# Kernel optimization log

Measured on AMD Instinct MI355X. Metric: run time of the kernel, lower is better.

Reference implementation:

```python
import jax, jax.numpy as jnp
import numpy as np

WINDOW = 2048
STEP = WINDOW // 2                 # 1024
N_SAMPLES = 131072
N_COEFFS = WINDOW // 2 + 1         # 1025
N_FRAMES = N_SAMPLES // STEP       # 128
Z_DIM = 128
BATCH, N_EVENTS, IMP_SAMPLES = 64, 1, 4096
BASE_RES = 0.02
RES_RANGE = (1.0 - BASE_RES) * 0.99


def setup_inputs() -> dict:
    key = jax.random.key(0)
    k1, k2, k3 = jax.random.split(key, 3)
    z = jax.random.normal(k1, (BATCH, N_EVENTS, Z_DIM), dtype=jnp.float32)
    impulse = jax.random.normal(k2, (BATCH, N_EVENTS, IMP_SAMPLES), dtype=jnp.float32)
    # stand-in for ConvUpsample: linear z -> (n_coeffs * n_frames)
    W_tf = jax.random.normal(k3, (Z_DIM, N_COEFFS * N_FRAMES), dtype=jnp.float32) * 0.02
    b_tf = jnp.zeros((N_COEFFS * N_FRAMES,), dtype=jnp.float32)
    return {"z": z, "impulse": impulse, "W_tf": W_tf, "b_tf": b_tf}


def _hann(n):
    # periodic hann (torch.hann_window default)
    return (0.5 - 0.5 * jnp.cos(2.0 * jnp.pi * jnp.arange(n) / n)).astype(jnp.float32)


def reference(z, impulse, W_tf, b_tf):
    B, E, imp_len = impulse.shape
    pad = N_SAMPLES - imp_len + WINDOW
    x = jnp.pad(impulse, ((0, 0), (0, 0), (0, pad)))  # (B,E,n_samples+window)
    win = _hann(WINDOW)

    # windowed_audio: overlapping frames * hann window -> (B,E,F,W)
    idx = jnp.arange(N_FRAMES)[:, None] * STEP + jnp.arange(WINDOW)[None, :]
    windowed = x[..., idx] * win

    # transfer functions: linear, reshape (C,F) -> transpose to (F,C), squash
    tf = (z.reshape(-1, Z_DIM) @ W_tf + b_tf).reshape(B, E, N_COEFFS, N_FRAMES)
    tf = jnp.transpose(tf, (0, 1, 3, 2))                       # (B,E,F,C)
    tf = BASE_RES + jax.nn.sigmoid(tf) * RES_RANGE

    cur_specs = jnp.fft.rfft(windowed, axis=-1)                # (B,E,F,C) complex64

    # advance_one_frame rotation: [re,im] @ [[c,-s],[s,-c]]
    g = jnp.linspace(0.0, np.pi, N_COEFFS).astype(jnp.float32)
    c, s = jnp.cos(g), jnp.sin(g)

    def step(prev_audio, inp):
        cur_spec, tfi = inp
        ps = jnp.fft.rfft(prev_audio, axis=-1)
        re, im = ps.real, ps.imag
        rot = jax.lax.complex(re * c + im * s, -(re * s + im * c))
        spec = (cur_spec + rot) * tfi
        audio = jnp.fft.irfft(spec, n=WINDOW, axis=-1)
        return audio, audio

    xs = (jnp.moveaxis(cur_specs, 2, 0), jnp.moveaxis(tf, 2, 0))
    init = jnp.zeros((B, E, WINDOW), dtype=jnp.float32)  # i==0: zero prev spec
    _, frames = jax.lax.scan(step, init, xs)             # (F,B,E,W)
    frames = jnp.moveaxis(frames, 0, 2) * win            # overlap_add apply_window=True

    # overlap-add with hop = WINDOW//2, vectorized via half-frame reshapes
    first = frames[..., :STEP].reshape(B, E, N_FRAMES * STEP)
    second = frames[..., STEP:].reshape(B, E, N_FRAMES * STEP)
    out = jnp.zeros((B, E, (N_FRAMES + 1) * STEP), dtype=jnp.float32)
    out = out.at[..., : N_FRAMES * STEP].add(first)
    out = out.at[..., STEP:].add(second)
    return out[..., :N_SAMPLES]
```

## Files before the change

### kernel.cpp

```cpp
#include <hip/hip_runtime.h>

#define NB 64
#define ZDIM 128
#define NCOEF 1025
#define NFR 128
#define COLS 131200
#define WINSZ 2048
#define HALFW 1024
#define NSAMP 131072
#define IMPN 4096
#define NCHUNK 32
#define NCK 31

#define TF_OFF   0
#define TF_SZ    (NB*COLS)
#define TFT_OFF  (TF_OFF + TF_SZ)
#define TFT_SZ   (NB*NFR*NCOEF)
#define CUR_OFF  (TFT_OFF + TFT_SZ)
#define CUR_SZ   (NB*4*NCOEF*2)
#define CK_OFF   (CUR_OFF + CUR_SZ)
#define CK_SZ    (NCK*NB*NCOEF*2)
#define WINT_OFF (CK_OFF + CK_SZ)
#define WINT_SZ  (WINSZ)
#define TW_OFF   (WINT_OFF + WINT_SZ)
#define TW_SZ    (HALFW*2)
#define ZBF_OFF  (TW_OFF + TW_SZ)
#define ZBF_SZ   (NB*ZDIM/2)

#define PHI(p) ((p) ^ ((((p) >> 4) & 3) << 2))

typedef short bf16x8 __attribute__((ext_vector_type(8)));
typedef float f32x4 __attribute__((ext_vector_type(4)));

__device__ __forceinline__ float2 cmul(float2 a, float2 b) {
  return make_float2(a.x * b.x - a.y * b.y, a.x * b.y + a.y * b.x);
}

#define WGBAR()                                              \
  do {                                                       \
    asm volatile("s_waitcnt lgkmcnt(0)" ::: "memory");       \
    __builtin_amdgcn_s_barrier();                            \
    asm volatile("" ::: "memory");                           \
  } while (0)

__device__ __forceinline__ short f2bf(float f) {
  unsigned u = __builtin_bit_cast(unsigned, f);
  u += 0x7FFFu + ((u >> 16) & 1u);
  return (short)(u >> 16);
}

__global__ __launch_bounds__(256) void init_tables(const float* __restrict__ z,
                                                   float* __restrict__ winT,
                                                   float2* __restrict__ twG,
                                                   short* __restrict__ zbf) {
  int i = blockIdx.x * 256 + threadIdx.x;
  if (i < WINSZ) {
    winT[i] = 0.5f - 0.5f * cosf((float)(2.0 * 3.14159265358979323846 / 2048.0) * (float)i);
  }
  if (i < HALFW) {
    float ang = (float)(-2.0 * 3.14159265358979323846 / 2048.0) * (float)i;
    float sv, cv;
    sincosf(ang, &sv, &cv);
    twG[i] = make_float2(cv, sv);
  }
  if (i < NB * ZDIM) zbf[i] = f2bf(z[i]);
}

__global__ __launch_bounds__(256, 2) void tf_gemm_mfma(const short* __restrict__ zbf,
                                                       const float* __restrict__ W,
                                                       const float* __restrict__ bias,
                                                       float* __restrict__ tf) {
  int tid = threadIdx.x;
  int wave = tid >> 6, lane = tid & 63;
  int colw = blockIdx.x * 128 + wave * 32;
  int lr = lane & 15;
  int lk = (lane >> 4) * 8;
  int lq = (lane >> 4) * 4;

  float wf[4][2][8];
#pragma unroll
  for (int s = 0; s < 4; ++s)
#pragma unroll
    for (int n = 0; n < 2; ++n) {
      const float* wp = W + (size_t)(s * 32 + lk) * COLS + colw + 16 * n + lr;
#pragma unroll
      for (int j = 0; j < 8; ++j)
        wf[s][n][j] = wp[(size_t)j * COLS];
    }

  bf16x8 afr[4][4];
#pragma unroll
  for (int s = 0; s < 4; ++s)
#pragma unroll
    for (int m = 0; m < 4; ++m)
      afr[s][m] = *reinterpret_cast<const bf16x8*>(zbf + (16 * m + lr) * ZDIM + s * 32 + lk);

  float bv[2];
#pragma unroll
  for (int n = 0; n < 2; ++n) bv[n] = bias[colw + 16 * n + lr];

  f32x4 acc[4][2];
#pragma unroll
  for (int m = 0; m < 4; ++m)
#pragma unroll
    for (int n = 0; n < 2; ++n)
      acc[m][n] = f32x4{bv[n], bv[n], bv[n], bv[n]};

#pragma unroll
  for (int s = 0; s < 4; ++s) {
    bf16x8 bfr[2];
#pragma unroll
    for (int n = 0; n < 2; ++n)
      bfr[n] = bf16x8{f2bf(wf[s][n][0]), f2bf(wf[s][n][1]), f2bf(wf[s][n][2]), f2bf(wf[s][n][3]),
                      f2bf(wf[s][n][4]), f2bf(wf[s][n][5]), f2bf(wf[s][n][6]), f2bf(wf[s][n][7])};
#pragma unroll
    for (int m = 0; m < 4; ++m)
#pragma unroll
      for (int n = 0; n < 2; ++n)
        acc[m][n] = __builtin_amdgcn_mfma_f32_16x16x32_bf16(afr[s][m], bfr[n], acc[m][n], 0, 0, 0);
  }

  const float RESR = (1.0f - 0.02f) * 0.99f;
#pragma unroll
  for (int n = 0; n < 2; ++n) {
    int col = colw + 16 * n + lr;
#pragma unroll
    for (int m = 0; m < 4; ++m) {
      int rowb = 16 * m + lq;
#pragma unroll
      for (int r = 0; r < 4; ++r) {
        float x = acc[m][n][r];
        float sg = 1.0f / (1.0f + __expf(-x));
        tf[(size_t)(rowb + r) * COLS + col] = 0.02f + sg * RESR;
      }
    }
  }
}

static __device__ __forceinline__ void wg_fft2048(float* ar, float* ai,
                                                  float* br, float* bi,
                                                  const float2* tw,
                                                  float** outr, float** outi) {
  float *xr = ar, *xi = ai, *yr = br, *yi = bi;
  int m = 1;
  for (int s = 0; s < 11; ++s) {
    __syncthreads();
#pragma unroll
    for (int it = 0; it < 4; ++it) {
      int t = (int)threadIdx.x + it * 256;
      int jm = t & ~(m - 1);
      float x0r = xr[t], x0i = xi[t];
      float x1r = xr[t + 1024], x1i = xi[t + 1024];
      float2 w = tw[jm];
      float sr = x0r + x1r, si = x0i + x1i;
      float dr = x0r - x1r, di = x0i - x1i;
      float pr = dr * w.x - di * w.y;
      float pi = dr * w.y + di * w.x;
      yr[t + jm] = sr;      yi[t + jm] = si;
      yr[t + jm + m] = pr;  yi[t + jm + m] = pi;
    }
    float* t0 = xr; xr = yr; yr = t0;
    float* t1 = xi; xi = yi; yi = t1;
    m <<= 1;
  }
  __syncthreads();
  *outr = xr; *outi = xi;
}

__global__ __launch_bounds__(256) void fwd_fft_kernel(const float* __restrict__ imp,
                                                      const float* __restrict__ winT,
                                                      const float2* __restrict__ twG,
                                                      float2* __restrict__ cur) {
  __shared__ float b0r[WINSZ], b0i[WINSZ], b1r[WINSZ], b1i[WINSZ];
  __shared__ float2 tw[HALFW];
  int wg = blockIdx.x;
  int b = wg >> 2, f = wg & 3;
  int tid = threadIdx.x;

  for (int i = tid; i < HALFW; i += 256) tw[i] = twG[i];
  for (int w = tid; w < WINSZ; w += 256) {
    int s = f * HALFW + w;
    float v = (s < IMPN) ? imp[(size_t)b * IMPN + s] * winT[w] : 0.0f;
    b0r[w] = v;
    b0i[w] = 0.0f;
  }
  float *rr, *ri;
  wg_fft2048(b0r, b0i, b1r, b1i, tw, &rr, &ri);
  for (int k = tid; k < NCOEF; k += 256)
    cur[(size_t)wg * NCOEF + k] = make_float2(rr[k], ri[k]);
}

__global__ __launch_bounds__(256) void recur_ck_t(const float* __restrict__ tf,
                                                  const float2* __restrict__ cur,
                                                  float2* __restrict__ ckp,
                                                  float* __restrict__ tft) {
  int id = blockIdx.x * 256 + threadIdx.x;
  if (id >= NB * NCOEF) return;
  int b = id / NCOEF;
  int k = id - b * NCOEF;

  float g = 3.14159265358979323846f * (float)k / 1024.0f;
  float sg, cg;
  sincosf(g, &sg, &cg);
  bool herm = (k == 0) || (k == HALFW);

  const float4* tf4 = (const float4*)(tf + (size_t)b * COLS + (size_t)k * NFR);
  const float2* curb = cur + (size_t)b * 4 * NCOEF + k;
  float* tftb = tft + (size_t)b * NFR * NCOEF + k;

  float pre = 0.0f, pim = 0.0f;
  for (int f4 = 0; f4 < 32; ++f4) {
    float4 tv = tf4[f4];
    float tfs[4] = {tv.x, tv.y, tv.z, tv.w};
#pragma unroll
    for (int u = 0; u < 4; ++u) {
      int f = 4 * f4 + u;
      tftb[(size_t)f * NCOEF] = tfs[u];
      if (f < 124) {
        float tfv = tfs[u];
        float cr = 0.0f, ci = 0.0f;
        if (f < 4) {
          float2 cv = curb[(size_t)f * NCOEF];
          cr = cv.x; ci = cv.y;
        }
        float ire = herm ? 0.0f : pim;
        float rre = fmaf(pre, cg, ire * sg);
        float rim = -fmaf(pre, sg, ire * cg);
        float sre = (cr + rre) * tfv;
        float sim = (ci + rim) * tfv;
        if ((f & 3) == 2)
          ckp[(size_t)((f - 2) >> 2) * NB * NCOEF + (size_t)b * NCOEF + k] = make_float2(sre, sim);
        pre = sre; pim = sim;
      }
    }
  }
}

__global__ __launch_bounds__(256) void fused_resyn(const float* __restrict__ tft,
                                                   const float2* __restrict__ cur,
                                                   const float2* __restrict__ ckp,
                                                   const float* __restrict__ winT,
                                                   const float2* __restrict__ twG,
                                                   float* __restrict__ out) {
  __shared__ float2 P[1024];
  __shared__ float2 Q[1024];

  int bidx = blockIdx.x;
  int b = bidx >> 5, c = bidx & 31;
  int t = threadIdx.x;

  float pre[5], pim[5], cgv[5], sgv[5];
#pragma unroll
  for (int i = 0; i < 5; ++i) {
    if (i == 4) { cgv[4] = -1.0f; sgv[4] = 0.0f; }
    else {
      float2 tv = twG[t + 256 * i];
      cgv[i] = tv.x; sgv[i] = -tv.y;
    }
    pre[i] = 0.0f; pim[i] = 0.0f;
  }
  if (c > 0) {
    const float2* ck = ckp + ((size_t)(c - 1) * NB + b) * NCOEF;
#pragma unroll
    for (int i = 0; i < 5; ++i) {
      if (i == 4 && t != 0) continue;
      int k = (i == 4) ? 1024 : t + 256 * i;
      float2 v = ck[k];
      pre[i] = v.x; pim[i] = v.y;
    }
  }

  float2 w1a = twG[2 * t];            float2 w1b = cmul(w1a, w1a); float2 w1c = cmul(w1b, w1a);
  float2 w2a = twG[8 * (t & 63)];     float2 w2b = cmul(w2a, w2a); float2 w2c = cmul(w2b, w2a);
  float2 w3a = twG[32 * (t & 15)];    float2 w3b = cmul(w3a, w3a); float2 w3c = cmul(w3b, w3a);
  float2 w4a = twG[128 * (t & 3)];    float2 w4b = cmul(w4a, w4a); float2 w4c = cmul(w4b, w4a);
  float2 twp0 = twG[t], twp1 = twG[t + 256], twp2 = twG[t + 512], twp3 = twG[t + 768];

  int mb = (t >> 6) + ((t >> 4) & 3) * 4 + ((t >> 2) & 3) * 16 + (t & 3) * 64;
  const float2* win2 = (const float2*)winT;
  float2 wv0 = win2[mb], wv1 = win2[mb + 256], wv2 = win2[mb + 512], wv3 = win2[mb + 768];

  int X0 = PHI(t);
  int B2 = 256 * (t >> 6) + ((t & 63) ^ (((t >> 4) & 3) << 2));
  int b3h = 64 * (t >> 4), i3 = t & 15;
  int b4h = 16 * (t >> 2), i4 = t & 3, c4 = (t >> 2) & 3;
  int p5 = b4h + 4 * ((t & 3) ^ c4);
  int pm0 = PHI((1024 - t) & 1023);
  int pm1 = PHI((1024 - (t + 256)) & 1023);
  int pm2 = PHI((1024 - (t + 512)) & 1023);
  int pm3 = PHI((1024 - (t + 768)) & 1023);

  const float* tftb = tft + (size_t)b * NFR * NCOEF;
  const float2* curb = cur + (size_t)b * 4 * NCOEF;
  const float Cs = 0.5f / 1024.0f;

  int fs = (c == 0) ? 0 : 4 * c - 1;
  int fe = 4 * c + 3;
  float carE0 = 0.0f, carO0 = 0.0f, carE1 = 0.0f, carO1 = 0.0f;

  float ntf[5];
  {
    const float* tfr = tftb + (size_t)fs * NCOEF;
#pragma unroll
    for (int i = 0; i < 4; ++i) ntf[i] = tfr[t + 256 * i];
    ntf[4] = (t == 0) ? tfr[1024] : 0.0f;
  }

  for (int f = fs; f <= fe; ++f) {
    float ctf[5];
#pragma unroll
    for (int i = 0; i < 5; ++i) ctf[i] = ntf[i];

    if (f < fe) {
      const float* tfr = tftb + (size_t)(f + 1) * NCOEF;
#pragma unroll
      for (int i = 0; i < 4; ++i) ntf[i] = tfr[t + 256 * i];
      ntf[4] = (t == 0) ? tfr[1024] : 0.0f;
    }

    float S[5], I[5];
#pragma unroll
    for (int i = 0; i < 5; ++i) {
      if (i == 4 && t != 0) { S[4] = 0.0f; I[4] = 0.0f; continue; }
      float cr = 0.0f, ci = 0.0f;
      if (f < 4) {
        int k = (i == 4) ? 1024 : t + 256 * i;
        float2 cv = curb[(size_t)f * NCOEF + k];
        cr = cv.x; ci = cv.y;
      }
      float rre = fmaf(pre[i], cgv[i], pim[i] * sgv[i]);
      float rim = -fmaf(pre[i], sgv[i], pim[i] * cgv[i]);
      S[i] = (cr + rre) * ctf[i];
      I[i] = (ci + rim) * ctf[i];
      pre[i] = S[i]; pim[i] = I[i];
    }

#pragma unroll
    for (int i = 0; i < 4; ++i)
      P[X0 + 256 * i] = make_float2(S[i], I[i]);
    WGBAR();

    float2 Z[4];
    {
      float2 xm[4];
      xm[0] = (t == 0) ? make_float2(S[4], 0.0f) : P[pm0];
      xm[1] = P[pm1]; xm[2] = P[pm2]; xm[3] = P[pm3];
      float2 twp[4] = {twp0, twp1, twp2, twp3};
#pragma unroll
      for (int i = 0; i < 4; ++i) {
        float xjr = S[i], xji = I[i];
        float cc = twp[i].x, sn = -twp[i].y;
        float Xer = Cs * (xjr + xm[i].x), Xei = Cs * (xji - xm[i].y);
        float Xpr = Cs * (xjr - xm[i].x), Xpi = Cs * (xji + xm[i].y);
        float Xor_ = Xpr * cc - Xpi * sn;
        float Xoi_ = Xpr * sn + Xpi * cc;
        Z[i] = make_float2(Xer - Xoi_, -(Xei + Xor_));
      }
    }
    float2 y0, y1, y2, y3;
    {
      float2 A = make_float2(Z[0].x + Z[2].x, Z[0].y + Z[2].y);
      float2 Bv = make_float2(Z[0].x - Z[2].x, Z[0].y - Z[2].y);
      float2 Cv = make_float2(Z[1].x + Z[3].x, Z[1].y + Z[3].y);
      float2 D = make_float2(Z[1].x - Z[3].x, Z[1].y - Z[3].y);
      y0 = make_float2(A.x + Cv.x, A.y + Cv.y);
      y1 = cmul(make_float2(Bv.x + D.y, Bv.y - D.x), w1a);
      y2 = cmul(make_float2(A.x - Cv.x, A.y - Cv.y), w1b);
      y3 = cmul(make_float2(Bv.x - D.y, Bv.y + D.x), w1c);
    }
    WGBAR();
    Q[X0]       = y0;
    Q[X0 + 256] = y1;
    Q[X0 + 512] = y2;
    Q[X0 + 768] = y3;
    WGBAR();

    float2 u0 = Q[B2], u1 = Q[B2 + 64], u2 = Q[B2 + 128], u3 = Q[B2 + 192];
    {
      float2 A = make_float2(u0.x + u2.x, u0.y + u2.y);
      float2 Bv = make_float2(u0.x - u2.x, u0.y - u2.y);
      float2 Cv = make_float2(u1.x + u3.x, u1.y + u3.y);
      float2 D = make_float2(u1.x - u3.x, u1.y - u3.y);
      Q[B2]       = make_float2(A.x + Cv.x, A.y + Cv.y);
      Q[B2 + 64]  = cmul(make_float2(Bv.x + D.y, Bv.y - D.x), w2a);
      Q[B2 + 128] = cmul(make_float2(A.x - Cv.x, A.y - Cv.y), w2b);
      Q[B2 + 192] = cmul(make_float2(Bv.x - D.y, Bv.y + D.x), w2c);
    }
    asm volatile("s_waitcnt lgkmcnt(0)" ::: "memory");

    u0 = Q[b3h + i3];
    u1 = Q[b3h + 16 + (i3 ^ 4)];
    u2 = Q[b3h + 32 + (i3 ^ 8)];
    u3 = Q[b3h + 48 + (i3 ^ 12)];
    {
      float2 A = make_float2(u0.x + u2.x, u0.y + u2.y);
      float2 Bv = make_float2(u0.x - u2.x, u0.y - u2.y);
      float2 Cv = make_float2(u1.x + u3.x, u1.y + u3.y);
      float2 D = make_float2(u1.x - u3.x, u1.y - u3.y);
      Q[b3h + i3]             = make_float2(A.x + Cv.x, A.y + Cv.y);
      Q[b3h + 16 + (i3 ^ 4)]  = cmul(make_float2(Bv.x + D.y, Bv.y - D.x), w3a);
      Q[b3h + 32 + (i3 ^ 8)]  = cmul(make_float2(A.x - Cv.x, A.y - Cv.y), w3b);
      Q[b3h + 48 + (i3 ^ 12)] = cmul(make_float2(Bv.x - D.y, Bv.y + D.x), w3c);
    }
    asm volatile("s_waitcnt lgkmcnt(0)" ::: "memory");

    u0 = Q[b4h + 4 * (0 ^ c4) + i4];
    u1 = Q[b4h + 4 * (1 ^ c4) + i4];
    u2 = Q[b4h + 4 * (2 ^ c4) + i4];
    u3 = Q[b4h + 4 * (3 ^ c4) + i4];
    {
      float2 A = make_float2(u0.x + u2.x, u0.y + u2.y);
      float2 Bv = make_float2(u0.x - u2.x, u0.y - u2.y);
      float2 Cv = make_float2(u1.x + u3.x, u1.y + u3.y);
      float2 D = make_float2(u1.x - u3.x, u1.y - u3.y);
      Q[b4h + 4 * (0 ^ c4) + i4] = make_float2(A.x + Cv.x, A.y + Cv.y);
      Q[b4h + 4 * (1 ^ c4) + i4] = cmul(make_float2(Bv.x + D.y, Bv.y - D.x), w4a);
      Q[b4h + 4 * (2 ^ c4) + i4] = cmul(make_float2(A.x - Cv.x, A.y - Cv.y), w4b);
      Q[b4h + 4 * (3 ^ c4) + i4] = cmul(make_float2(Bv.x - D.y, Bv.y + D.x), w4c);
    }
    asm volatile("s_waitcnt lgkmcnt(0)" ::: "memory");

    float4 q01 = *reinterpret_cast<const float4*>(&Q[p5]);
    float4 q23 = *reinterpret_cast<const float4*>(&Q[p5 + 2]);
    float2 z0, z1, z2, z3;
    {
      float2 a = make_float2(q01.x, q01.y), bq = make_float2(q01.z, q01.w);
      float2 cq = make_float2(q23.x, q23.y), d = make_float2(q23.z, q23.w);
      float2 A = make_float2(a.x + cq.x, a.y + cq.y);
      float2 Bv = make_float2(a.x - cq.x, a.y - cq.y);
      float2 Cv = make_float2(bq.x + d.x, bq.y + d.y);
      float2 D = make_float2(bq.x - d.x, bq.y - d.y);
      z0 = make_float2(A.x + Cv.x, A.y + Cv.y);
      z1 = make_float2(Bv.x + D.y, Bv.y - D.x);
      z2 = make_float2(A.x - Cv.x, A.y - Cv.y);
      z3 = make_float2(Bv.x - D.y, Bv.y + D.x);
    }

    float e0 = z0.x * wv0.x, o0 = -z0.y * wv0.y;
    float e1 = z1.x * wv1.x, o1 = -z1.y * wv1.y;
    float e2 = z2.x * wv2.x, o2 = -z2.y * wv2.y;
    float e3 = z3.x * wv3.x, o3 = -z3.y * wv3.y;
    if (f >= 4 * c) {
      float2* ob2 = (float2*)(out + (size_t)b * NSAMP + (size_t)f * 1024);
      ob2[mb]       = make_float2(e0 + carE0, o0 + carO0);
      ob2[mb + 256] = make_float2(e1 + carE1, o1 + carO1);
    }
    carE0 = e2; carO0 = o2;
    carE1 = e3; carO1 = o3;
  }
}

extern "C" void kernel_launch(void* const* d_in, const int* in_sizes, int n_in,
                              void* d_out, int out_size, void* d_ws, size_t ws_size,
                              hipStream_t stream) {
  const float* z    = (const float*)d_in[0];
  const float* imp  = (const float*)d_in[1];
  const float* W    = (const float*)d_in[2];
  const float* bias = (const float*)d_in[3];

  float* ws = (float*)d_ws;
  float*  tf   = ws + TF_OFF;
  float*  tft  = ws + TFT_OFF;
  float2* cur  = (float2*)(ws + CUR_OFF);
  float2* ckp  = (float2*)(ws + CK_OFF);
  float*  winT = ws + WINT_OFF;
  float2* twG  = (float2*)(ws + TW_OFF);
  short*  zbf  = (short*)(ws + ZBF_OFF);
  float*  out  = (float*)d_out;

  init_tables<<<32, 256, 0, stream>>>(z, winT, twG, zbf);
  tf_gemm_mfma<<<COLS / 128, 256, 0, stream>>>(zbf, W, bias, tf);
  fwd_fft_kernel<<<NB * 4, 256, 0, stream>>>(imp, winT, twG, cur);
  recur_ck_t<<<(NB * NCOEF + 255) / 256, 256, 0, stream>>>(tf, cur, ckp, tft);
  fused_resyn<<<NB * NCHUNK, 256, 0, stream>>>(tft, cur, ckp, winT, twG, out);
}
```

Measured before the change: 93.97 us.

## Stage GEMM weights via LDS async loads; recompute FFT twiddles to cut registers

The transfer-function GEMM now stages its 128x128 weight tile into shared memory with global_load_lds direct copies instead of holding 64 floats per thread in registers. A-fragments are loaded per k-step rather than all upfront, and the launch-bounds occupancy hint is dropped. In the FFT recurrence kernel, derived twiddles (squares, cubes, quarter-rotations) are recomputed each frame from a few base values pinned by empty asm, trading extra ALU work for lower register pressure. The likely aim is higher occupancy or fewer spills in both kernels.

```diff
diff --git a/kernel.cpp b/kernel.cpp
--- a/kernel.cpp
+++ b/kernel.cpp
@@ -49,6 +49,12 @@
   return (short)(u >> 16);
 }
 
+__device__ __forceinline__ void gload_lds16(const float* g, float* l) {
+  __builtin_amdgcn_global_load_lds(
+      (const __attribute__((address_space(1))) unsigned int*)(const void*)g,
+      (__attribute__((address_space(3))) unsigned int*)(void*)l, 16, 0, 0);
+}
+
 __global__ __launch_bounds__(256) void init_tables(const float* __restrict__ z,
                                                    float* __restrict__ winT,
                                                    float2* __restrict__ twG,
@@ -66,34 +72,26 @@
   if (i < NB * ZDIM) zbf[i] = f2bf(z[i]);
 }
 
-__global__ __launch_bounds__(256, 2) void tf_gemm_mfma(const short* __restrict__ zbf,
-                                                       const float* __restrict__ W,
-                                                       const float* __restrict__ bias,
-                                                       float* __restrict__ tf) {
+__global__ __launch_bounds__(256) void tf_gemm_mfma(const short* __restrict__ zbf,
+                                                    const float* __restrict__ W,
+                                                    const float* __restrict__ bias,
+                                                    float* __restrict__ tf) {
+  __shared__ float Wt[128 * 128];
   int tid = threadIdx.x;
   int wave = tid >> 6, lane = tid & 63;
-  int colw = blockIdx.x * 128 + wave * 32;
+  int colb = blockIdx.x * 128;
+
+#pragma unroll
+  for (int it = 0; it < 16; ++it) {
+    int cq = wave * 16 + it;
+    const float* src = W + (size_t)(2 * cq + (lane >> 5)) * COLS + colb + (lane & 31) * 4;
+    gload_lds16(src, &Wt[cq * 256]);
+  }
+
   int lr = lane & 15;
   int lk = (lane >> 4) * 8;
   int lq = (lane >> 4) * 4;
-
-  float wf[4][2][8];
-#pragma unroll
-  for (int s = 0; s < 4; ++s)
-#pragma unroll
-    for (int n = 0; n < 2; ++n) {
-      const float* wp = W + (size_t)(s * 32 + lk) * COLS + colw + 16 * n + lr;
-#pragma unroll
-      for (int j = 0; j < 8; ++j)
-        wf[s][n][j] = wp[(size_t)j * COLS];
-    }
-
-  bf16x8 afr[4][4];
-#pragma unroll
-  for (int s = 0; s < 4; ++s)
-#pragma unroll
-    for (int m = 0; m < 4; ++m)
-      afr[s][m] = *reinterpret_cast<const bf16x8*>(zbf + (16 * m + lr) * ZDIM + s * 32 + lk);
+  int colw = colb + wave * 32;
 
   float bv[2];
 #pragma unroll
@@ -106,18 +104,26 @@
     for (int n = 0; n < 2; ++n)
       acc[m][n] = f32x4{bv[n], bv[n], bv[n], bv[n]};
 
+  __syncthreads();
+
 #pragma unroll
   for (int s = 0; s < 4; ++s) {
+    bf16x8 afr[4];
+#pragma unroll
+    for (int m = 0; m < 4; ++m)
+      afr[m] = *reinterpret_cast<const bf16x8*>(zbf + (16 * m + lr) * ZDIM + s * 32 + lk);
     bf16x8 bfr[2];
 #pragma unroll
-    for (int n = 0; n < 2; ++n)
-      bfr[n] = bf16x8{f2bf(wf[s][n][0]), f2bf(wf[s][n][1]), f2bf(wf[s][n][2]), f2bf(wf[s][n][3]),
-                      f2bf(wf[s][n][4]), f2bf(wf[s][n][5]), f2bf(wf[s][n][6]), f2bf(wf[s][n][7])};
+    for (int n = 0; n < 2; ++n) {
+      const float* wp = &Wt[(s * 32 + lk) * 128 + wave * 32 + 16 * n + lr];
+      bfr[n] = bf16x8{f2bf(wp[0 * 128]), f2bf(wp[1 * 128]), f2bf(wp[2 * 128]), f2bf(wp[3 * 128]),
+                      f2bf(wp[4 * 128]), f2bf(wp[5 * 128]), f2bf(wp[6 * 128]), f2bf(wp[7 * 128])};
+    }
 #pragma unroll
     for (int m = 0; m < 4; ++m)
 #pragma unroll
       for (int n = 0; n < 2; ++n)
-        acc[m][n] = __builtin_amdgcn_mfma_f32_16x16x32_bf16(afr[s][m], bfr[n], acc[m][n], 0, 0, 0);
+        acc[m][n] = __builtin_amdgcn_mfma_f32_16x16x32_bf16(afr[m], bfr[n], acc[m][n], 0, 0, 0);
   }
 
   const float RESR = (1.0f - 0.02f) * 0.99f;
@@ -270,11 +276,11 @@
     }
   }
 
-  float2 w1a = twG[2 * t];            float2 w1b = cmul(w1a, w1a); float2 w1c = cmul(w1b, w1a);
-  float2 w2a = twG[8 * (t & 63)];     float2 w2b = cmul(w2a, w2a); float2 w2c = cmul(w2b, w2a);
-  float2 w3a = twG[32 * (t & 15)];    float2 w3b = cmul(w3a, w3a); float2 w3c = cmul(w3b, w3a);
-  float2 w4a = twG[128 * (t & 3)];    float2 w4b = cmul(w4a, w4a); float2 w4c = cmul(w4b, w4a);
-  float2 twp0 = twG[t], twp1 = twG[t + 256], twp2 = twG[t + 512], twp3 = twG[t + 768];
+  float2 w1a = twG[2 * t];
+  float2 w2a = twG[8 * (t & 63)];
+  float2 w3a = twG[32 * (t & 15)];
+  float2 w4a = twG[128 * (t & 3)];
+  float2 twp0 = twG[t];
 
   int mb = (t >> 6) + ((t >> 4) & 3) * 4 + ((t >> 2) & 3) * 16 + (t & 3) * 64;
   const float2* win2 = (const float2*)winT;
@@ -306,7 +312,13 @@
     ntf[4] = (t == 0) ? tfr[1024] : 0.0f;
   }
 
+#define KEEP(x) asm volatile("" : "+v"(x))
+
   for (int f = fs; f <= fe; ++f) {
+    KEEP(w1a.x); KEEP(w1a.y); KEEP(w2a.x); KEEP(w2a.y);
+    KEEP(w3a.x); KEEP(w3a.y); KEEP(w4a.x); KEEP(w4a.y);
+    KEEP(twp0.x); KEEP(twp0.y);
+
     float ctf[5];
 #pragma unroll
     for (int i = 0; i < 5; ++i) ctf[i] = ntf[i];
@@ -340,6 +352,10 @@
       P[X0 + 256 * i] = make_float2(S[i], I[i]);
     WGBAR();
 
+    const float R2 = 0.70710678118654752f;
+    float2 twp1 = cmul(twp0, make_float2(R2, -R2));
+    float2 twp2 = make_float2(twp0.y, -twp0.x);
+    float2 twp3 = make_float2(twp1.y, -twp1.x);
     float2 Z[4];
     {
       float2 xm[4];
@@ -359,6 +375,8 @@
     }
     float2 y0, y1, y2, y3;
     {
+      float2 w1b = cmul(w1a, w1a);
+      float2 w1c = cmul(w1b, w1a);
       float2 A = make_float2(Z[0].x + Z[2].x, Z[0].y + Z[2].y);
       float2 Bv = make_float2(Z[0].x - Z[2].x, Z[0].y - Z[2].y);
       float2 Cv = make_float2(Z[1].x + Z[3].x, Z[1].y + Z[3].y);
@@ -377,6 +395,8 @@
 
     float2 u0 = Q[B2], u1 = Q[B2 + 64], u2 = Q[B2 + 128], u3 = Q[B2 + 192];
     {
+      float2 w2b = cmul(w2a, w2a);
+      float2 w2c = cmul(w2b, w2a);
       float2 A = make_float2(u0.x + u2.x, u0.y + u2.y);
       float2 Bv = make_float2(u0.x - u2.x, u0.y - u2.y);
       float2 Cv = make_float2(u1.x + u3.x, u1.y + u3.y);
@@ -393,6 +413,8 @@
     u2 = Q[b3h + 32 + (i3 ^ 8)];
     u3 = Q[b3h + 48 + (i3 ^ 12)];
     {
+      float2 w3b = cmul(w3a, w3a);
+      float2 w3c = cmul(w3b, w3a);
       float2 A = make_float2(u0.x + u2.x, u0.y + u2.y);
       float2 Bv = make_float2(u0.x - u2.x, u0.y - u2.y);
       float2 Cv = make_float2(u1.x + u3.x, u1.y + u3.y);
@@ -409,6 +431,8 @@
     u2 = Q[b4h + 4 * (2 ^ c4) + i4];
     u3 = Q[b4h + 4 * (3 ^ c4) + i4];
     {
+      float2 w4b = cmul(w4a, w4a);
+      float2 w4c = cmul(w4b, w4a);
       float2 A = make_float2(u0.x + u2.x, u0.y + u2.y);
       float2 Bv = make_float2(u0.x - u2.x, u0.y - u2.y);
       float2 Cv = make_float2(u1.x + u3.x, u1.y + u3.y);
@@ -448,6 +472,7 @@
     carE0 = e2; carO0 = o2;
     carE1 = e3; carO1 = o3;
   }
+#undef KEEP
 }
 
 extern "C" void kernel_launch(void* const* d_in, const int* in_sizes, int n_in,
```

Result: slower. 97.97 us (+4.3%).
